# Performance work log

Hardware: AMD Instinct MI355X
Metric: run time of the kernel (lower is better)

The kernel has to match this reference:

```python
import jax, jax.numpy as jnp
import numpy as np


def _leaky(x):
    return jnp.where(x > 0, x, 0.2 * x)


def _time_warp(x, strength, k_wp, k_sh):
    # Vectorized equivalent of the per-sample python loop in _apply_time_warp.
    B, L, Fd = x.shape
    warp_steps = (L * 0.1 * strength).astype(jnp.int32)
    wp = jax.random.randint(k_wp, (B, 1), warp_steps, L - warp_steps)
    sh = jax.random.randint(k_sh, (B, 1), -warp_steps, warp_steps + 1)
    t = jnp.arange(L)[None, :]
    # shift > 0: warped[t] = x[min(t+shift, L-1)] for t >= warp_point, else x[t]
    pos = jnp.where(t >= wp, jnp.minimum(t + sh, L - 1), t)
    # shift < 0: warped[t] = x[t - shift] for warp_point+shift <= t < L+shift, else x[t]
    neg = jnp.where((t >= wp + sh) & (t < L + sh), t - sh, t)
    idx = jnp.where(sh > 0, pos, jnp.where(sh < 0, neg, t))  # (B, L)
    warped = x[jnp.arange(B)[:, None], idx]  # gather along time -> (B, L, Fd)
    return warped


def _freq_aug(x, strength, k_f):
    fx = jnp.fft.fft(x, axis=1)
    ratio = jnp.minimum(strength * 0.1, 0.5)
    keep = jax.random.uniform(k_f, x.shape) > ratio
    res = jnp.fft.ifft(fx * keep.astype(fx.dtype), axis=1).real.astype(x.dtype)
    return jnp.where(strength < 0.01, x, res)


def _forward(x, batch_size, w1, b1, w2, b2, w3, b3, wm, bm, wn, bn, ws, bs,
             p_mask, p_noise, p_shift, p_scale):
    B, L, Fd = x.shape
    s_mask = jax.nn.sigmoid(p_mask)
    s_noise = jax.nn.sigmoid(p_noise)
    s_shift = jax.nn.sigmoid(p_shift)
    s_scale = jax.nn.sigmoid(p_scale)
    s_mix = 1.0 - s_shift

    key = jax.random.key(42)
    kz, kn, kwp, ksh, kf = jax.random.split(key, 5)

    z = jax.random.normal(kz, (B, w1.shape[0]), x.dtype)
    h = _leaky(z @ w1 + b1)
    h = _leaky(h @ w2 + b2)
    h = _leaky(h @ w3 + b3)  # (B, 2*hidden)

    mask = jax.nn.sigmoid(h @ wm + bm).reshape(B, L, Fd)
    mask = 1.0 - (1.0 - mask) * s_mask * 0.3

    noise_mag = jax.nn.softplus(h @ wn + bn).reshape(B, L, Fd)
    noise = jax.random.normal(kn, x.shape, x.dtype) * noise_mag * s_noise * 0.05

    warped = _time_warp(x, s_shift, kwp, ksh)

    scale = jax.nn.softplus(h @ ws + bs)[:, None, :]  # (B,1,Fd)
    scale = 1.0 + (scale - 0.5) * 0.2 * s_scale

    freq = _freq_aug(x, s_mix, kf)

    wa = jnp.clip(1.0 - s_mix - s_shift, 0.1, 0.8)
    wb = s_mix * 0.5
    wc = s_shift * 0.5
    tot = wa + wb + wc
    wa, wb, wc = wa / tot, wb / tot, wc / tot

    aug = x * mask * scale + noise
    aug = aug * wa + freq * wb + warped * wc
    return aug


def setup_inputs() -> dict:
    key = jax.random.key(0)
    ks = jax.random.split(key, 8)
    B, L, Fd = 256, 512, 64
    H, ND = 128, 64
    x = jax.random.normal(ks[0], (B, L, Fd), jnp.float32)

    def lin(k, i, o):
        return jax.random.normal(k, (i, o), jnp.float32) * 0.02

    inp = {
        "x": x,
        "batch_size": B,
        "w1": lin(ks[1], ND, H), "b1": jnp.zeros((H,), jnp.float32),
        "w2": lin(ks[2], H, 2 * H), "b2": jnp.zeros((2 * H,), jnp.float32),
        "w3": lin(ks[3], 2 * H, 2 * H), "b3": jnp.zeros((2 * H,), jnp.float32),
        "wm": lin(ks[4], 2 * H, L * Fd), "bm": jnp.zeros((L * Fd,), jnp.float32),
        "wn": lin(ks[5], 2 * H, L * Fd), "bn": jnp.zeros((L * Fd,), jnp.float32),
        "ws": lin(ks[6], 2 * H, Fd), "bs": jnp.zeros((Fd,), jnp.float32),
        "p_mask": jnp.float32(0.5), "p_noise": jnp.float32(0.5),
        "p_shift": jnp.float32(0.5), "p_scale": jnp.float32(0.5),
    }
    return inp


def reference(x, batch_size, w1, b1, w2, b2, w3, b3, wm, bm, wn, bn, ws, bs,
              p_mask, p_noise, p_shift, p_scale):
    return _forward(x, batch_size, w1, b1, w2, b2, w3, b3, wm, bm, wn, bn,
                    ws, bs, p_mask, p_noise, p_shift, p_scale)
```

## Files before the change

### kernel.cpp

```cpp
#include <hip/hip_runtime.h>
#include <cstdint>
#include <cstddef>


typedef unsigned int u32;
typedef unsigned short u16;

#define Bd 256
#define Ld 512
#define Fd 64
#define Nd 32768

struct U2 { u32 a, b; };

__device__ __forceinline__ u32 rotl32(u32 x, int r){ return (x << r) | (x >> (32 - r)); }

__device__ __forceinline__ U2 tf2x32(u32 k0, u32 k1, u32 x0, u32 x1){
  u32 ks2 = k0 ^ k1 ^ 0x1BD11BDAu;
  x0 += k0; x1 += k1;
#define TFR4(r0,r1,r2,r3) \
  x0 += x1; x1 = rotl32(x1, r0); x1 ^= x0; \
  x0 += x1; x1 = rotl32(x1, r1); x1 ^= x0; \
  x0 += x1; x1 = rotl32(x1, r2); x1 ^= x0; \
  x0 += x1; x1 = rotl32(x1, r3); x1 ^= x0;
  TFR4(13,15,26,6)  x0 += k1;  x1 += ks2 + 1u;
  TFR4(17,29,16,24) x0 += ks2; x1 += k0 + 2u;
  TFR4(13,15,26,6)  x0 += k0;  x1 += k1 + 3u;
  TFR4(17,29,16,24) x0 += k1;  x1 += ks2 + 4u;
  TFR4(13,15,26,6)  x0 += ks2; x1 += k0 + 5u;
#undef TFR4
  U2 r; r.a = x0; r.b = x1; return r;
}

__device__ __forceinline__ u32 rb32(u32 k0, u32 k1, u32 i){
  U2 r = tf2x32(k0, k1, 0u, i);
  return r.a ^ r.b;
}

__device__ __forceinline__ U2 split_key(u32 k0, u32 k1, u32 j){
  return tf2x32(k0, k1, 0u, j);
}

__device__ __forceinline__ float sigmoidf_(float x){ return 1.0f / (1.0f + expf(-x)); }
__device__ __forceinline__ float softplusf_(float x){ return fmaxf(x, 0.0f) + log1pf(expf(-fabsf(x))); }
__device__ __forceinline__ float leakyf_(float x){ return (x > 0.0f) ? x : 0.2f * x; }

__device__ __forceinline__ float erfinvf_(float x){
  float w = -log1pf(-x * x);
  float p;
  if (w < 5.0f){
    w -= 2.5f;
    p =               2.81022636e-08f;
    p = fmaf(p, w,    3.43273939e-07f);
    p = fmaf(p, w,   -3.5233877e-06f);
    p = fmaf(p, w,   -4.39150654e-06f);
    p = fmaf(p, w,    0.00021858087f);
    p = fmaf(p, w,   -0.00125372503f);
    p = fmaf(p, w,   -0.00417768164f);
    p = fmaf(p, w,    0.246640727f);
    p = fmaf(p, w,    1.50140941f);
  } else {
    w = sqrtf(w) - 3.0f;
    p =              -0.000200214257f;
    p = fmaf(p, w,    0.000100950558f);
    p = fmaf(p, w,    0.00134934322f);
    p = fmaf(p, w,   -0.00367342844f);
    p = fmaf(p, w,    0.00573950773f);
    p = fmaf(p, w,   -0.0076224613f);
    p = fmaf(p, w,    0.00943887047f);
    p = fmaf(p, w,    1.00167406f);
    p = fmaf(p, w,    2.83297682f);
  }
  return p * x;
}

__device__ __forceinline__ float uniform_from_bits(u32 bits){
  return __uint_as_float((bits >> 9) | 0x3f800000u) - 1.0f;
}

__device__ __forceinline__ float normal_from_bits(u32 bits){
  float u01 = uniform_from_bits(bits);
  const float lo = -0.99999994f;
  float v = fmaf(u01, 2.0f, lo);
  v = fmaxf(lo, v);
  return 1.41421356f * erfinvf_(v);
}

__device__ __forceinline__ int warp_idx_(int t, int wp, int sh){
  int tps = t + sh;
  int pos = (t >= wp) ? ((tps < Ld - 1) ? tps : (Ld - 1)) : t;
  int neg = ((t >= wp + sh) && (t < Ld + sh)) ? (t - sh) : t;
  return (sh > 0) ? pos : ((sh < 0) ? neg : t);
}

__device__ __forceinline__ u32 pack_bf16_2(float a, float b){
  u32 ua = __float_as_uint(a), ub = __float_as_uint(b);
  u32 ra = (ua + 0x7FFFu + ((ua >> 16) & 1u)) >> 16;
  u32 rb = (ub + 0x7FFFu + ((ub >> 16) & 1u)) >> 16;
  return (ra & 0xFFFFu) | (rb << 16);
}
__device__ __forceinline__ u16 f2bf(float a){
  u32 ua = __float_as_uint(a);
  return (u16)((ua + 0x7FFFu + ((ua >> 16) & 1u)) >> 16);
}
__device__ __forceinline__ float bf2f(u16 v){
  return __uint_as_float(((u32)v) << 16);
}

__device__ __forceinline__ int swz_(int v){
  return ((v >> 2) & 7) ^ ((v & 3) << 1);
}
__device__ __forceinline__ int rev9_(int k){
  return (int)(__brev((u32)k) >> 23);
}

__global__ __launch_bounds__(256) void k_mlp(
    const float* __restrict__ w1, const float* __restrict__ b1,
    const float* __restrict__ w2, const float* __restrict__ b2,
    const float* __restrict__ w3, const float* __restrict__ b3,
    const float* __restrict__ wsc, const float* __restrict__ bsc,
    const float* __restrict__ p_scale, const float* __restrict__ p_shift,
    u16* __restrict__ h3b, float* __restrict__ scl,
    int* __restrict__ wp, int* __restrict__ shv)
{
  __shared__ float zs[64];
  __shared__ float h1s[128];
  __shared__ float h2s[256];
  __shared__ float hs[256];
  int b = blockIdx.x, n = threadIdx.x;

  if (n < 64){
    U2 kz = split_key(0u, 42u, 0u);
    zs[n] = normal_from_bits(rb32(kz.a, kz.b, (u32)(b * 64 + n)));
  }
  __syncthreads();

  if (n < 128){
    float acc = b1[n];
    #pragma unroll 8
    for (int k = 0; k < 64; ++k) acc = fmaf(zs[k], w1[k * 128 + n], acc);
    h1s[n] = leakyf_(acc);
  }
  __syncthreads();

  {
    float acc = b2[n];
    #pragma unroll 8
    for (int k = 0; k < 128; ++k) acc = fmaf(h1s[k], w2[k * 256 + n], acc);
    h2s[n] = leakyf_(acc);
  }
  __syncthreads();

  {
    float acc = b3[n];
    #pragma unroll 8
    for (int k = 0; k < 256; ++k) acc = fmaf(h2s[k], w3[k * 256 + n], acc);
    u16 hv = f2bf(leakyf_(acc));
    h3b[b * 256 + n] = hv;
    hs[n] = bf2f(hv);
  }
  __syncthreads();

  if (n < 64){
    float a2 = bsc[n];
    for (int k = 0; k < 256; ++k) a2 = fmaf(hs[k], wsc[k * 64 + n], a2);
    float s_scale = sigmoidf_(p_scale[0]);
    scl[b * 64 + n] = 1.0f + (softplusf_(a2) - 0.5f) * 0.2f * s_scale;
  }

  if (b < 2 && n < 128){
    int bb = b * 128 + n;
    float s_shift = sigmoidf_(p_shift[0]);
    int wsteps = (int)(51.2f * s_shift);
    U2 kwp = split_key(0u, 42u, 2u);
    U2 ksh = split_key(0u, 42u, 3u);
    {
      U2 k1 = split_key(kwp.a, kwp.b, 0u);
      U2 k2 = split_key(kwp.a, kwp.b, 1u);
      u32 hi = rb32(k1.a, k1.b, (u32)bb);
      u32 lo = rb32(k2.a, k2.b, (u32)bb);
      u32 span = (u32)(Ld - 2 * wsteps);
      u32 mult = 65536u % span; mult = (mult * mult) % span;
      u32 off = ((hi % span) * mult + (lo % span)) % span;
      wp[bb] = wsteps + (int)off;
    }
    {
      U2 k1 = split_key(ksh.a, ksh.b, 0u);
      U2 k2 = split_key(ksh.a, ksh.b, 1u);
      u32 hi = rb32(k1.a, k1.b, (u32)bb);
      u32 lo = rb32(k2.a, k2.b, (u32)bb);
      u32 span = (u32)(2 * wsteps + 1);
      u32 mult = 65536u % span; mult = (mult * mult) % span;
      u32 off = ((hi % span) * mult + (lo % span)) % span;
      shv[bb] = -wsteps + (int)off;
    }
  }
}

typedef short short8 __attribute__((ext_vector_type(8)));
typedef float f32x4 __attribute__((ext_vector_type(4)));
union Frag { uint4 u; short8 s; };

__global__ __launch_bounds__(256, 2) void k_gemm(
    const u16* __restrict__ h3b,
    const float* __restrict__ wm, const float* __restrict__ bm,
    const float* __restrict__ wn, const float* __restrict__ bn,
    u32* __restrict__ mn)
{
  __shared__ __align__(16) u32 As [128 * 32];
  __shared__ __align__(16) u32 Bs0[128 * 32];
  __shared__ __align__(16) u32 Bs1[128 * 32];

  const int tid  = threadIdx.x;
  const int lane = tid & 63;
  const int w    = tid >> 6;
  const int q    = lane >> 4;
  const int lo   = lane & 15;
  const int nt0  = blockIdx.x << 7;
  const int b0   = blockIdx.y << 7;
  const int wr   = (w >> 1) << 6;
  const int wc   = (w & 1) << 6;

  const int p  = lane >> 3;
  const int c8 = lane & 7;
  const int nb = (w << 5) + (p << 2);

  f32x4 accm[4][4], accn[4][4];
  #pragma unroll
  for (int i = 0; i < 4; ++i)
    #pragma unroll
    for (int j = 0; j < 4; ++j){ accm[i][j] = (f32x4)0.0f; accn[i][j] = (f32x4)0.0f; }

  for (int kc = 0; kc < 256; kc += 64){
    if (kc) __syncthreads();
    #pragma unroll
    for (int j = 0; j < 4; ++j){
      int idx  = j * 256 + tid;
      int row  = idx >> 3;
      int slot = idx & 7;
      int g    = slot ^ swz_(row);
      uint4 v  = *(const uint4*)(h3b + (size_t)(b0 + row) * 256 + kc + g * 8);
      *(uint4*)&As[row * 32 + slot * 4] = v;
    }
    #pragma unroll
    for (int cp = 0; cp < 4; ++cp){
      int c = cp * 8 + c8;
      size_t gb = (size_t)(kc + 2 * c) * Nd + nt0 + nb;
      float4 m0 = *(const float4*)(wm + gb);
      float4 m1 = *(const float4*)(wm + gb + Nd);
      float4 v0 = *(const float4*)(wn + gb);
      float4 v1 = *(const float4*)(wn + gb + Nd);
      int g = c >> 2, cl = c & 3;
      #pragma unroll
      for (int s = 0; s < 4; ++s){
        int n = nb + s;
        int addr = n * 32 + (g ^ swz_(n)) * 4 + cl;
        float a0 = (s == 0) ? m0.x : (s == 1) ? m0.y : (s == 2) ? m0.z : m0.w;
        float a1 = (s == 0) ? m1.x : (s == 1) ? m1.y : (s == 2) ? m1.z : m1.w;
        float b0f = (s == 0) ? v0.x : (s == 1) ? v0.y : (s == 2) ? v0.z : v0.w;
        float b1f = (s == 0) ? v1.x : (s == 1) ? v1.y : (s == 2) ? v1.z : v1.w;
        Bs0[addr] = pack_bf16_2(a0, a1);
        Bs1[addr] = pack_bf16_2(b0f, b1f);
      }
    }
    __syncthreads();

    #pragma unroll
    for (int u = 0; u < 2; ++u){
      int G = u * 4 + q;
      Frag af[4], bfm[4], bfn[4];
      #pragma unroll
      for (int mt = 0; mt < 4; ++mt){
        int row = wr + mt * 16 + lo;
        af[mt].u = *(const uint4*)&As[row * 32 + (G ^ swz_(row)) * 4];
      }
      #pragma unroll
      for (int nt = 0; nt < 4; ++nt){
        int n = wc + nt * 16 + lo;
        int ad = n * 32 + (G ^ swz_(n)) * 4;
        bfm[nt].u = *(const uint4*)&Bs0[ad];
        bfn[nt].u = *(const uint4*)&Bs1[ad];
      }
      #pragma unroll
      for (int mt = 0; mt < 4; ++mt){
        #pragma unroll
        for (int nt = 0; nt < 4; ++nt){
          accm[mt][nt] = __builtin_amdgcn_mfma_f32_16x16x32_bf16(af[mt].s, bfm[nt].s, accm[mt][nt], 0, 0, 0);
          accn[mt][nt] = __builtin_amdgcn_mfma_f32_16x16x32_bf16(af[mt].s, bfn[nt].s, accn[mt][nt], 0, 0, 0);
        }
      }
    }
  }

  #pragma unroll
  for (int nt = 0; nt < 4; ++nt){
    int n = nt0 + wc + nt * 16 + lo;
    float bmv = bm[n];
    float bnv = bn[n];
    #pragma unroll
    for (int mt = 0; mt < 4; ++mt){
      #pragma unroll
      for (int r = 0; r < 4; ++r){
        int b = b0 + wr + mt * 16 + q * 4 + r;
        size_t o = (size_t)b * Nd + n;
        mn[o] = pack_bf16_2(accm[mt][nt][r] + bmv, accn[mt][nt][r] + bnv);
      }
    }
  }
}

__global__ __launch_bounds__(256) void k_noise(u32* __restrict__ mn,
                                               const float* __restrict__ p_noise){
  int gid = blockIdx.x * 256 + threadIdx.x;
  u32 base = (u32)gid * 8u;
  float s_noise = sigmoidf_(p_noise[0]);
  float sc = s_noise * 0.05f;
  U2 knk = split_key(0u, 42u, 1u);

  uint4 v0 = *(const uint4*)(mn + base);
  uint4 v1 = *(const uint4*)(mn + base + 4);
  u32 wds[8] = {v0.x, v0.y, v0.z, v0.w, v1.x, v1.y, v1.z, v1.w};
  #pragma unroll
  for (int h = 0; h < 8; ++h){
    u16 logit = (u16)(wds[h] >> 16);
    float nm = softplusf_(bf2f(logit));
    float nz = normal_from_bits(rb32(knk.a, knk.b, base + (u32)h));
    wds[h] = (wds[h] & 0xFFFFu) | ((u32)f2bf(nz * nm * sc) << 16);
  }
  *(uint4*)(mn + base)     = make_uint4(wds[0], wds[1], wds[2], wds[3]);
  *(uint4*)(mn + base + 4) = make_uint4(wds[4], wds[5], wds[6], wds[7]);
}

#define PITCH 529

__device__ __forceinline__ int lphys(int t){ return t + (t >> 5); }

__global__ __launch_bounds__(256, 4) void k_faug(
    const float* __restrict__ x,
    u32* mn,
    const float* __restrict__ scl,
    const int* __restrict__ wp, const int* __restrict__ shv,
    const float* __restrict__ p_mask, const float* __restrict__ p_noise,
    const float* __restrict__ p_shift)
{
  __shared__ float SR[8 * PITCH];
  __shared__ float SI[8 * PITCH];
  __shared__ float2 tw[256];

  const int tid = threadIdx.x;
  const int b   = blockIdx.x >> 2;
  const int f0  = (blockIdx.x & 3) << 4;

  float s_mask  = sigmoidf_(p_mask[0]);
  float s_shift = sigmoidf_(p_shift[0]);
  float s_mix   = 1.0f - s_shift;
  float ratio   = fminf(s_mix * 0.1f, 0.5f);
  float wa = 1.0f - s_mix - s_shift;
  wa = fminf(fmaxf(wa, 0.1f), 0.8f);
  float wb = s_mix * 0.5f;
  float wc = s_shift * 0.5f;
  float tot = wa + wb + wc;
  wa /= tot; wb /= tot; wc /= tot;
  bool pass = (s_mix < 0.01f);
  (void)p_noise;

  U2 kf  = split_key(0u, 42u, 4u);
  const int wpb = wp[b];
  const int shb = shv[b];

  {
    float ang = -6.283185307179586f * ((float)tid / 512.0f);
    tw[tid] = make_float2(cosf(ang), sinf(ang));
  }

  const float* xb = x + (size_t)b * Nd;
  #pragma unroll
  for (int s = 0; s < 8; ++s){
    int qq = (s << 8) + tid;
    int t  = qq >> 2;
    int f4 = qq & 3;
    float4 v = *(const float4*)(xb + t * 64 + f0 + (f4 << 2));
    int j = f4 << 1;
    int pt = lphys(t);
    SR[j * PITCH + pt]       = v.x;  SI[j * PITCH + pt]       = v.y;
    SR[(j + 1) * PITCH + pt] = v.z;  SI[(j + 1) * PITCH + pt] = v.w;
  }
  __syncthreads();

  for (int s = 9; s >= 1; --s){
    int half = 1 << (s - 1);
    #pragma unroll
    for (int it = 0; it < 8; ++it){
      int j  = it;
      int bi = tid;
      int pos = bi & (half - 1);
      int g = bi >> (s - 1);
      int i1 = (g << s) + pos;
      int i2 = i1 + half;
      int a1 = j * PITCH + lphys(i1);
      int a2 = j * PITCH + lphys(i2);
      float ur = SR[a1], ui = SI[a1];
      float vr = SR[a2], vi = SI[a2];
      SR[a1] = ur + vr; SI[a1] = ui + vi;
      float dr = ur - vr, di = ui - vi;
      float2 w = tw[pos << (9 - s)];
      SR[a2] = dr * w.x - di * w.y;
      SI[a2] = dr * w.y + di * w.x;
    }
    __syncthreads();
  }

  #pragma unroll
  for (int it = 0; it < 8; ++it){
    int j = it;
    int k = tid;
    int nItr = (k == 0) ? 2 : 1;
    for (int e = 0; e < nItr; ++e){
      int kk = (e == 0) ? k : 256;
      int nk = (512 - kk) & 511;
      int pk = rev9_(kk), pn = rev9_(nk);
      int ak = j * PITCH + lphys(pk);
      int an = j * PITCH + lphys(pn);
      float zkr = SR[ak], zki = SI[ak];
      float znr = SR[an], zni = SI[an];
      float X0r = 0.5f * (zkr + znr), X0i = 0.5f * (zki - zni);
      float X1r = 0.5f * (zki + zni), X1i = 0.5f * (znr - zkr);
      int fA = f0 + (j << 1);
      u32 ck = (u32)((b * Ld + kk) * Fd + fA);
      u32 cn = (u32)((b * Ld + nk) * Fd + fA);
      float k0a = (uniform_from_bits(rb32(kf.a, kf.b, ck))      > ratio) ? 1.0f : 0.0f;
      float k0b = (uniform_from_bits(rb32(kf.a, kf.b, cn))      > ratio) ? 1.0f : 0.0f;
      float k1a = (uniform_from_bits(rb32(kf.a, kf.b, ck + 1u)) > ratio) ? 1.0f : 0.0f;
      float k1b = (uniform_from_bits(rb32(kf.a, kf.b, cn + 1u)) > ratio) ? 1.0f : 0.0f;
      float m0 = 0.5f * (k0a + k0b);
      float m1 = 0.5f * (k1a + k1b);
      SR[ak] = m0 * X0r - m1 * X1i;
      SI[ak] = m0 * X0i + m1 * X1r;
      SR[an] = m0 * X0r + m1 * X1i;
      SI[an] = m1 * X1r - m0 * X0i;
    }
  }
  __syncthreads();

  for (int s = 1; s <= 9; ++s){
    int half = 1 << (s - 1);
    #pragma unroll
    for (int it = 0; it < 8; ++it){
      int j  = it;
      int bi = tid;
      int pos = bi & (half - 1);
      int g = bi >> (s - 1);
      int i1 = (g << s) + pos;
      int i2 = i1 + half;
      int a1 = j * PITCH + lphys(i1);
      int a2 = j * PITCH + lphys(i2);
      float2 w = tw[pos << (9 - s)];
      float vr = SR[a2], vi = SI[a2];
      float tx_ = vr * w.x + vi * w.y;
      float ty_ = vi * w.x - vr * w.y;
      float ur = SR[a1], ui = SI[a1];
      SR[a1] = ur + tx_; SI[a1] = ui + ty_;
      SR[a2] = ur - tx_; SI[a2] = ui - ty_;
    }
    __syncthreads();
  }

  const float inv512 = 1.0f / 512.0f;
  u32* mnb = mn + (size_t)b * Nd;
  #pragma unroll
  for (int s = 0; s < 8; ++s){
    int qq = (s << 8) + tid;
    int t  = qq >> 2;
    int f4 = qq & 3;
    int f  = f0 + (f4 << 2);
    int j  = f4 << 1;
    int pt = lphys(t);
    int nidx = t * 64 + f;
    float4 xv = *(const float4*)(xb + nidx);
    int wi = warp_idx_(t, wpb, shb);
    float4 wv = *(const float4*)(xb + wi * 64 + f);
    float4 sc = *(const float4*)(scl + b * 64 + f);
    uint4 w4 = *(const uint4*)(mnb + nidx);
    float fr[4];
    fr[0] = SR[j * PITCH + pt] * inv512;
    fr[1] = SI[j * PITCH + pt] * inv512;
    fr[2] = SR[(j + 1) * PITCH + pt] * inv512;
    fr[3] = SI[(j + 1) * PITCH + pt] * inv512;
    const float xvv[4] = {xv.x, xv.y, xv.z, xv.w};
    const float wvv[4] = {wv.x, wv.y, wv.z, wv.w};
    const float scv[4] = {sc.x, sc.y, sc.z, sc.w};
    const u32 wdv[4] = {w4.x, w4.y, w4.z, w4.w};
    float o[4];
    #pragma unroll
    for (int c = 0; c < 4; ++c){
      float maskv = sigmoidf_(bf2f((u16)(wdv[c] & 0xFFFFu)));
      maskv = 1.0f - (1.0f - maskv) * s_mask * 0.3f;
      float noise = bf2f((u16)(wdv[c] >> 16));
      float fq = pass ? xvv[c] : fr[c];
      float aug = fmaf(xvv[c] * maskv, scv[c], noise);
      o[c] = aug * wa + fq * wb + wvv[c] * wc;
    }
    *(float4*)(mnb + nidx) = make_float4(o[0], o[1], o[2], o[3]);
  }
}

extern "C" void kernel_launch(void* const* d_in, const int* in_sizes, int n_in,
                              void* d_out, int out_size, void* d_ws, size_t ws_size,
                              hipStream_t stream)
{
  (void)in_sizes; (void)n_in; (void)out_size; (void)ws_size;
  const float* x   = (const float*)d_in[0];
  const float* w1  = (const float*)d_in[2];
  const float* b1  = (const float*)d_in[3];
  const float* w2  = (const float*)d_in[4];
  const float* b2  = (const float*)d_in[5];
  const float* w3  = (const float*)d_in[6];
  const float* b3  = (const float*)d_in[7];
  const float* wm  = (const float*)d_in[8];
  const float* bm  = (const float*)d_in[9];
  const float* wn  = (const float*)d_in[10];
  const float* bn  = (const float*)d_in[11];
  const float* wsc = (const float*)d_in[12];
  const float* bsc = (const float*)d_in[13];
  const float* pm  = (const float*)d_in[14];
  const float* pn  = (const float*)d_in[15];
  const float* psh = (const float*)d_in[16];
  const float* psc = (const float*)d_in[17];
  char* ws = (char*)d_ws;

  int*   wp   = (int*)(ws + 0);
  int*   shv  = (int*)(ws + 1024);
  u16*   h3b  = (u16*)(ws + 4096);
  float* scl  = (float*)(ws + 4096 + 131072);
  u32*   mn   = (u32*)d_out;

  k_mlp  <<<dim3(256),     dim3(256), 0, stream>>>(w1, b1, w2, b2, w3, b3,
                                                   wsc, bsc, psc, psh,
                                                   h3b, scl, wp, shv);
  k_gemm <<<dim3(256, 2),  dim3(256), 0, stream>>>(h3b, wm, bm, wn, bn, mn);
  k_noise<<<dim3(4096),    dim3(256), 0, stream>>>(mn, pn);
  k_faug <<<dim3(1024),    dim3(256), 0, stream>>>(x, mn, scl, wp, shv,
                                                   pm, pn, psh);
}
```

Before: 315.3 us.

## Fuse all four kernels into one cooperative persistent kernel with grid syncs

Replaces the four separate launches (MLP, GEMM, noise, frequency augmentation) with a single cooperative kernel. Each phase iterates over its work items with a persistent grid-stride loop, and phases are separated by grid.sync(), with shared memory reused across phases. The goal is to remove launch overhead and inter-kernel gaps. In exchange, occupancy is capped at what a cooperative launch allows, the 1024 FFT tiles and 4096 noise blocks now run on fewer resident blocks, and grid-wide barriers add their own cost.

```diff
diff --git a/kernel.cpp b/kernel.cpp
--- a/kernel.cpp
+++ b/kernel.cpp
@@ -1,6 +1,9 @@
 #include <hip/hip_runtime.h>
+#include <hip/hip_cooperative_groups.h>
 #include <cstdint>
 #include <cstddef>
+
+namespace cg = cooperative_groups;
 
 
 typedef unsigned int u32;
@@ -114,393 +117,401 @@
   return (int)(__brev((u32)k) >> 23);
 }
 
-__global__ __launch_bounds__(256) void k_mlp(
+typedef short short8 __attribute__((ext_vector_type(8)));
+typedef float f32x4 __attribute__((ext_vector_type(4)));
+union Frag { uint4 u; short8 s; };
+
+#define PITCH 529
+__device__ __forceinline__ int lphys(int t){ return t + (t >> 5); }
+
+__global__ __launch_bounds__(256, 2) void k_mega(
+    const float* __restrict__ x,
     const float* __restrict__ w1, const float* __restrict__ b1,
     const float* __restrict__ w2, const float* __restrict__ b2,
     const float* __restrict__ w3, const float* __restrict__ b3,
-    const float* __restrict__ wsc, const float* __restrict__ bsc,
-    const float* __restrict__ p_scale, const float* __restrict__ p_shift,
-    u16* __restrict__ h3b, float* __restrict__ scl,
-    int* __restrict__ wp, int* __restrict__ shv)
-{
-  __shared__ float zs[64];
-  __shared__ float h1s[128];
-  __shared__ float h2s[256];
-  __shared__ float hs[256];
-  int b = blockIdx.x, n = threadIdx.x;
-
-  if (n < 64){
-    U2 kz = split_key(0u, 42u, 0u);
-    zs[n] = normal_from_bits(rb32(kz.a, kz.b, (u32)(b * 64 + n)));
-  }
-  __syncthreads();
-
-  if (n < 128){
-    float acc = b1[n];
-    #pragma unroll 8
-    for (int k = 0; k < 64; ++k) acc = fmaf(zs[k], w1[k * 128 + n], acc);
-    h1s[n] = leakyf_(acc);
-  }
-  __syncthreads();
-
-  {
-    float acc = b2[n];
-    #pragma unroll 8
-    for (int k = 0; k < 128; ++k) acc = fmaf(h1s[k], w2[k * 256 + n], acc);
-    h2s[n] = leakyf_(acc);
-  }
-  __syncthreads();
-
-  {
-    float acc = b3[n];
-    #pragma unroll 8
-    for (int k = 0; k < 256; ++k) acc = fmaf(h2s[k], w3[k * 256 + n], acc);
-    u16 hv = f2bf(leakyf_(acc));
-    h3b[b * 256 + n] = hv;
-    hs[n] = bf2f(hv);
-  }
-  __syncthreads();
-
-  if (n < 64){
-    float a2 = bsc[n];
-    for (int k = 0; k < 256; ++k) a2 = fmaf(hs[k], wsc[k * 64 + n], a2);
-    float s_scale = sigmoidf_(p_scale[0]);
-    scl[b * 64 + n] = 1.0f + (softplusf_(a2) - 0.5f) * 0.2f * s_scale;
-  }
-
-  if (b < 2 && n < 128){
-    int bb = b * 128 + n;
-    float s_shift = sigmoidf_(p_shift[0]);
-    int wsteps = (int)(51.2f * s_shift);
-    U2 kwp = split_key(0u, 42u, 2u);
-    U2 ksh = split_key(0u, 42u, 3u);
-    {
-      U2 k1 = split_key(kwp.a, kwp.b, 0u);
-      U2 k2 = split_key(kwp.a, kwp.b, 1u);
-      u32 hi = rb32(k1.a, k1.b, (u32)bb);
-      u32 lo = rb32(k2.a, k2.b, (u32)bb);
-      u32 span = (u32)(Ld - 2 * wsteps);
-      u32 mult = 65536u % span; mult = (mult * mult) % span;
-      u32 off = ((hi % span) * mult + (lo % span)) % span;
-      wp[bb] = wsteps + (int)off;
-    }
-    {
-      U2 k1 = split_key(ksh.a, ksh.b, 0u);
-      U2 k2 = split_key(ksh.a, ksh.b, 1u);
-      u32 hi = rb32(k1.a, k1.b, (u32)bb);
-      u32 lo = rb32(k2.a, k2.b, (u32)bb);
-      u32 span = (u32)(2 * wsteps + 1);
-      u32 mult = 65536u % span; mult = (mult * mult) % span;
-      u32 off = ((hi % span) * mult + (lo % span)) % span;
-      shv[bb] = -wsteps + (int)off;
-    }
-  }
-}
-
-typedef short short8 __attribute__((ext_vector_type(8)));
-typedef float f32x4 __attribute__((ext_vector_type(4)));
-union Frag { uint4 u; short8 s; };
-
-__global__ __launch_bounds__(256, 2) void k_gemm(
-    const u16* __restrict__ h3b,
     const float* __restrict__ wm, const float* __restrict__ bm,
     const float* __restrict__ wn, const float* __restrict__ bn,
-    u32* __restrict__ mn)
+    const float* __restrict__ wsc, const float* __restrict__ bsc,
+    const float* __restrict__ pm, const float* __restrict__ pn,
+    const float* __restrict__ psh, const float* __restrict__ psc,
+    u16* __restrict__ h3b, float* __restrict__ scl,
+    int* __restrict__ wp, int* __restrict__ shv,
+    u32* mn)
 {
-  __shared__ __align__(16) u32 As [128 * 32];
-  __shared__ __align__(16) u32 Bs0[128 * 32];
-  __shared__ __align__(16) u32 Bs1[128 * 32];
-
-  const int tid  = threadIdx.x;
-  const int lane = tid & 63;
-  const int w    = tid >> 6;
-  const int q    = lane >> 4;
-  const int lo   = lane & 15;
-  const int nt0  = blockIdx.x << 7;
-  const int b0   = blockIdx.y << 7;
-  const int wr   = (w >> 1) << 6;
-  const int wc   = (w & 1) << 6;
-
-  const int p  = lane >> 3;
-  const int c8 = lane & 7;
-  const int nb = (w << 5) + (p << 2);
-
-  f32x4 accm[4][4], accn[4][4];
-  #pragma unroll
-  for (int i = 0; i < 4; ++i)
-    #pragma unroll
-    for (int j = 0; j < 4; ++j){ accm[i][j] = (f32x4)0.0f; accn[i][j] = (f32x4)0.0f; }
-
-  for (int kc = 0; kc < 256; kc += 64){
-    if (kc) __syncthreads();
-    #pragma unroll
-    for (int j = 0; j < 4; ++j){
-      int idx  = j * 256 + tid;
-      int row  = idx >> 3;
-      int slot = idx & 7;
-      int g    = slot ^ swz_(row);
-      uint4 v  = *(const uint4*)(h3b + (size_t)(b0 + row) * 256 + kc + g * 8);
-      *(uint4*)&As[row * 32 + slot * 4] = v;
-    }
-    #pragma unroll
-    for (int cp = 0; cp < 4; ++cp){
-      int c = cp * 8 + c8;
-      size_t gb = (size_t)(kc + 2 * c) * Nd + nt0 + nb;
-      float4 m0 = *(const float4*)(wm + gb);
-      float4 m1 = *(const float4*)(wm + gb + Nd);
-      float4 v0 = *(const float4*)(wn + gb);
-      float4 v1 = *(const float4*)(wn + gb + Nd);
-      int g = c >> 2, cl = c & 3;
+  cg::grid_group grid = cg::this_grid();
+  __shared__ __align__(16) u32 SMEM[12288];
+
+  const int bid = blockIdx.x;
+  const int tid = threadIdx.x;
+  const int gsz = gridDim.x;
+
+  for (int b = bid; b < 256; b += gsz){
+    float* zs  = (float*)SMEM;
+    float* h1s = zs + 64;
+    float* h2s = h1s + 128;
+    float* hs  = h2s + 256;
+    int n = tid;
+    __syncthreads();
+
+    if (n < 64){
+      U2 kz = split_key(0u, 42u, 0u);
+      zs[n] = normal_from_bits(rb32(kz.a, kz.b, (u32)(b * 64 + n)));
+    }
+    __syncthreads();
+
+    if (n < 128){
+      float acc = b1[n];
+      #pragma unroll 8
+      for (int k = 0; k < 64; ++k) acc = fmaf(zs[k], w1[k * 128 + n], acc);
+      h1s[n] = leakyf_(acc);
+    }
+    __syncthreads();
+
+    {
+      float acc = b2[n];
+      #pragma unroll 8
+      for (int k = 0; k < 128; ++k) acc = fmaf(h1s[k], w2[k * 256 + n], acc);
+      h2s[n] = leakyf_(acc);
+    }
+    __syncthreads();
+
+    {
+      float acc = b3[n];
+      #pragma unroll 8
+      for (int k = 0; k < 256; ++k) acc = fmaf(h2s[k], w3[k * 256 + n], acc);
+      u16 hv = f2bf(leakyf_(acc));
+      h3b[b * 256 + n] = hv;
+      hs[n] = bf2f(hv);
+    }
+    __syncthreads();
+
+    if (n < 64){
+      float a2 = bsc[n];
+      for (int k = 0; k < 256; ++k) a2 = fmaf(hs[k], wsc[k * 64 + n], a2);
+      float s_scale = sigmoidf_(psc[0]);
+      scl[b * 64 + n] = 1.0f + (softplusf_(a2) - 0.5f) * 0.2f * s_scale;
+    }
+
+    if (b < 2 && n < 128){
+      int bb = b * 128 + n;
+      float s_shift = sigmoidf_(psh[0]);
+      int wsteps = (int)(51.2f * s_shift);
+      U2 kwp = split_key(0u, 42u, 2u);
+      U2 ksh = split_key(0u, 42u, 3u);
+      {
+        U2 k1 = split_key(kwp.a, kwp.b, 0u);
+        U2 k2 = split_key(kwp.a, kwp.b, 1u);
+        u32 hi = rb32(k1.a, k1.b, (u32)bb);
+        u32 lo = rb32(k2.a, k2.b, (u32)bb);
+        u32 span = (u32)(Ld - 2 * wsteps);
+        u32 mult = 65536u % span; mult = (mult * mult) % span;
+        u32 off = ((hi % span) * mult + (lo % span)) % span;
+        wp[bb] = wsteps + (int)off;
+      }
+      {
+        U2 k1 = split_key(ksh.a, ksh.b, 0u);
+        U2 k2 = split_key(ksh.a, ksh.b, 1u);
+        u32 hi = rb32(k1.a, k1.b, (u32)bb);
+        u32 lo = rb32(k2.a, k2.b, (u32)bb);
+        u32 span = (u32)(2 * wsteps + 1);
+        u32 mult = 65536u % span; mult = (mult * mult) % span;
+        u32 off = ((hi % span) * mult + (lo % span)) % span;
+        shv[bb] = -wsteps + (int)off;
+      }
+    }
+  }
+  grid.sync();
+
+  {
+    u32* As  = SMEM;
+    u32* Bs0 = SMEM + 4096;
+    u32* Bs1 = SMEM + 8192;
+
+    const int lane = tid & 63;
+    const int w    = tid >> 6;
+    const int q    = lane >> 4;
+    const int lo   = lane & 15;
+    const int wr   = (w >> 1) << 6;
+    const int wc   = (w & 1) << 6;
+
+    const int p  = lane >> 3;
+    const int c8 = lane & 7;
+    const int nb = (w << 5) + (p << 2);
+
+    for (int tile = bid; tile < 512; tile += gsz){
+      const int nt0 = (tile & 255) << 7;
+      const int b0  = (tile >> 8) << 7;
+
+      f32x4 accm[4][4], accn[4][4];
       #pragma unroll
-      for (int s = 0; s < 4; ++s){
-        int n = nb + s;
-        int addr = n * 32 + (g ^ swz_(n)) * 4 + cl;
-        float a0 = (s == 0) ? m0.x : (s == 1) ? m0.y : (s == 2) ? m0.z : m0.w;
-        float a1 = (s == 0) ? m1.x : (s == 1) ? m1.y : (s == 2) ? m1.z : m1.w;
-        float b0f = (s == 0) ? v0.x : (s == 1) ? v0.y : (s == 2) ? v0.z : v0.w;
-        float b1f = (s == 0) ? v1.x : (s == 1) ? v1.y : (s == 2) ? v1.z : v1.w;
-        Bs0[addr] = pack_bf16_2(a0, a1);
-        Bs1[addr] = pack_bf16_2(b0f, b1f);
-      }
-    }
-    __syncthreads();
-
-    #pragma unroll
-    for (int u = 0; u < 2; ++u){
-      int G = u * 4 + q;
-      Frag af[4], bfm[4], bfn[4];
-      #pragma unroll
-      for (int mt = 0; mt < 4; ++mt){
-        int row = wr + mt * 16 + lo;
-        af[mt].u = *(const uint4*)&As[row * 32 + (G ^ swz_(row)) * 4];
-      }
+      for (int i = 0; i < 4; ++i)
+        #pragma unroll
+        for (int j = 0; j < 4; ++j){ accm[i][j] = (f32x4)0.0f; accn[i][j] = (f32x4)0.0f; }
+
+      for (int kc = 0; kc < 256; kc += 64){
+        __syncthreads();
+        #pragma unroll
+        for (int j = 0; j < 4; ++j){
+          int idx  = j * 256 + tid;
+          int row  = idx >> 3;
+          int slot = idx & 7;
+          int g    = slot ^ swz_(row);
+          uint4 v  = *(const uint4*)(h3b + (size_t)(b0 + row) * 256 + kc + g * 8);
+          *(uint4*)&As[row * 32 + slot * 4] = v;
+        }
+        #pragma unroll
+        for (int cp = 0; cp < 4; ++cp){
+          int c = cp * 8 + c8;
+          size_t gb = (size_t)(kc + 2 * c) * Nd + nt0 + nb;
+          float4 m0 = *(const float4*)(wm + gb);
+          float4 m1 = *(const float4*)(wm + gb + Nd);
+          float4 v0 = *(const float4*)(wn + gb);
+          float4 v1 = *(const float4*)(wn + gb + Nd);
+          int g = c >> 2, cl = c & 3;
+          #pragma unroll
+          for (int s = 0; s < 4; ++s){
+            int n = nb + s;
+            int addr = n * 32 + (g ^ swz_(n)) * 4 + cl;
+            float a0 = (s == 0) ? m0.x : (s == 1) ? m0.y : (s == 2) ? m0.z : m0.w;
+            float a1 = (s == 0) ? m1.x : (s == 1) ? m1.y : (s == 2) ? m1.z : m1.w;
+            float b0f = (s == 0) ? v0.x : (s == 1) ? v0.y : (s == 2) ? v0.z : v0.w;
+            float b1f = (s == 0) ? v1.x : (s == 1) ? v1.y : (s == 2) ? v1.z : v1.w;
+            Bs0[addr] = pack_bf16_2(a0, a1);
+            Bs1[addr] = pack_bf16_2(b0f, b1f);
+          }
+        }
+        __syncthreads();
+
+        #pragma unroll
+        for (int u = 0; u < 2; ++u){
+          int G = u * 4 + q;
+          Frag af[4], bfm[4], bfn[4];
+          #pragma unroll
+          for (int mt = 0; mt < 4; ++mt){
+            int row = wr + mt * 16 + lo;
+            af[mt].u = *(const uint4*)&As[row * 32 + (G ^ swz_(row)) * 4];
+          }
+          #pragma unroll
+          for (int nt = 0; nt < 4; ++nt){
+            int n = wc + nt * 16 + lo;
+            int ad = n * 32 + (G ^ swz_(n)) * 4;
+            bfm[nt].u = *(const uint4*)&Bs0[ad];
+            bfn[nt].u = *(const uint4*)&Bs1[ad];
+          }
+          #pragma unroll
+          for (int mt = 0; mt < 4; ++mt){
+            #pragma unroll
+            for (int nt = 0; nt < 4; ++nt){
+              accm[mt][nt] = __builtin_amdgcn_mfma_f32_16x16x32_bf16(af[mt].s, bfm[nt].s, accm[mt][nt], 0, 0, 0);
+              accn[mt][nt] = __builtin_amdgcn_mfma_f32_16x16x32_bf16(af[mt].s, bfn[nt].s, accn[mt][nt], 0, 0, 0);
+            }
+          }
+        }
+      }
+
       #pragma unroll
       for (int nt = 0; nt < 4; ++nt){
-        int n = wc + nt * 16 + lo;
-        int ad = n * 32 + (G ^ swz_(n)) * 4;
-        bfm[nt].u = *(const uint4*)&Bs0[ad];
-        bfn[nt].u = *(const uint4*)&Bs1[ad];
-      }
+        int n = nt0 + wc + nt * 16 + lo;
+        float bmv = bm[n];
+        float bnv = bn[n];
+        #pragma unroll
+        for (int mt = 0; mt < 4; ++mt){
+          #pragma unroll
+          for (int r = 0; r < 4; ++r){
+            int b = b0 + wr + mt * 16 + q * 4 + r;
+            size_t o = (size_t)b * Nd + n;
+            mn[o] = pack_bf16_2(accm[mt][nt][r] + bmv, accn[mt][nt][r] + bnv);
+          }
+        }
+      }
+    }
+  }
+  grid.sync();
+
+  {
+    float s_noise = sigmoidf_(pn[0]);
+    float sc = s_noise * 0.05f;
+    U2 knk = split_key(0u, 42u, 1u);
+    for (int nb2 = bid; nb2 < 4096; nb2 += gsz){
+      int gid = nb2 * 256 + tid;
+      u32 base = (u32)gid * 8u;
+      uint4 v0 = *(const uint4*)(mn + base);
+      uint4 v1 = *(const uint4*)(mn + base + 4);
+      u32 wds[8] = {v0.x, v0.y, v0.z, v0.w, v1.x, v1.y, v1.z, v1.w};
       #pragma unroll
-      for (int mt = 0; mt < 4; ++mt){
-        #pragma unroll
-        for (int nt = 0; nt < 4; ++nt){
-          accm[mt][nt] = __builtin_amdgcn_mfma_f32_16x16x32_bf16(af[mt].s, bfm[nt].s, accm[mt][nt], 0, 0, 0);
-          accn[mt][nt] = __builtin_amdgcn_mfma_f32_16x16x32_bf16(af[mt].s, bfn[nt].s, accn[mt][nt], 0, 0, 0);
-        }
-      }
+      for (int h = 0; h < 8; ++h){
+        u16 logit = (u16)(wds[h] >> 16);
+        float nm = softplusf_(bf2f(logit));
+        float nz = normal_from_bits(rb32(knk.a, knk.b, base + (u32)h));
+        wds[h] = (wds[h] & 0xFFFFu) | ((u32)f2bf(nz * nm * sc) << 16);
+      }
+      *(uint4*)(mn + base)     = make_uint4(wds[0], wds[1], wds[2], wds[3]);
+      *(uint4*)(mn + base + 4) = make_uint4(wds[4], wds[5], wds[6], wds[7]);
     }
   }
-
-  #pragma unroll
-  for (int nt = 0; nt < 4; ++nt){
-    int n = nt0 + wc + nt * 16 + lo;
-    float bmv = bm[n];
-    float bnv = bn[n];
-    #pragma unroll
-    for (int mt = 0; mt < 4; ++mt){
+  grid.sync();
+
+  {
+    float*  SR = (float*)SMEM;
+    float*  SI = SR + 8 * PITCH;
+    float2* tw = (float2*)(SI + 8 * PITCH);
+
+    float s_mask  = sigmoidf_(pm[0]);
+    float s_shift = sigmoidf_(psh[0]);
+    float s_mix   = 1.0f - s_shift;
+    float ratio   = fminf(s_mix * 0.1f, 0.5f);
+    float wa = 1.0f - s_mix - s_shift;
+    wa = fminf(fmaxf(wa, 0.1f), 0.8f);
+    float wb = s_mix * 0.5f;
+    float wc = s_shift * 0.5f;
+    float tot = wa + wb + wc;
+    wa /= tot; wb /= tot; wc /= tot;
+    bool pass = (s_mix < 0.01f);
+
+    U2 kf = split_key(0u, 42u, 4u);
+
+    {
+      float ang = -6.283185307179586f * ((float)tid / 512.0f);
+      tw[tid] = make_float2(cosf(ang), sinf(ang));
+    }
+
+    for (int tile = bid; tile < 1024; tile += gsz){
+      const int b  = tile >> 2;
+      const int f0 = (tile & 3) << 4;
+      const int wpb = wp[b];
+      const int shb = shv[b];
+      __syncthreads();
+
+      const float* xb = x + (size_t)b * Nd;
       #pragma unroll
-      for (int r = 0; r < 4; ++r){
-        int b = b0 + wr + mt * 16 + q * 4 + r;
-        size_t o = (size_t)b * Nd + n;
-        mn[o] = pack_bf16_2(accm[mt][nt][r] + bmv, accn[mt][nt][r] + bnv);
-      }
-    }
-  }
-}
-
-__global__ __launch_bounds__(256) void k_noise(u32* __restrict__ mn,
-                                               const float* __restrict__ p_noise){
-  int gid = blockIdx.x * 256 + threadIdx.x;
-  u32 base = (u32)gid * 8u;
-  float s_noise = sigmoidf_(p_noise[0]);
-  float sc = s_noise * 0.05f;
-  U2 knk = split_key(0u, 42u, 1u);
-
-  uint4 v0 = *(const uint4*)(mn + base);
-  uint4 v1 = *(const uint4*)(mn + base + 4);
-  u32 wds[8] = {v0.x, v0.y, v0.z, v0.w, v1.x, v1.y, v1.z, v1.w};
-  #pragma unroll
-  for (int h = 0; h < 8; ++h){
-    u16 logit = (u16)(wds[h] >> 16);
-    float nm = softplusf_(bf2f(logit));
-    float nz = normal_from_bits(rb32(knk.a, knk.b, base + (u32)h));
-    wds[h] = (wds[h] & 0xFFFFu) | ((u32)f2bf(nz * nm * sc) << 16);
-  }
-  *(uint4*)(mn + base)     = make_uint4(wds[0], wds[1], wds[2], wds[3]);
-  *(uint4*)(mn + base + 4) = make_uint4(wds[4], wds[5], wds[6], wds[7]);
-}
-
-#define PITCH 529
-
-__device__ __forceinline__ int lphys(int t){ return t + (t >> 5); }
-
-__global__ __launch_bounds__(256, 4) void k_faug(
-    const float* __restrict__ x,
-    u32* mn,
-    const float* __restrict__ scl,
-    const int* __restrict__ wp, const int* __restrict__ shv,
-    const float* __restrict__ p_mask, const float* __restrict__ p_noise,
-    const float* __restrict__ p_shift)
-{
-  __shared__ float SR[8 * PITCH];
-  __shared__ float SI[8 * PITCH];
-  __shared__ float2 tw[256];
-
-  const int tid = threadIdx.x;
-  const int b   = blockIdx.x >> 2;
-  const int f0  = (blockIdx.x & 3) << 4;
-
-  float s_mask  = sigmoidf_(p_mask[0]);
-  float s_shift = sigmoidf_(p_shift[0]);
-  float s_mix   = 1.0f - s_shift;
-  float ratio   = fminf(s_mix * 0.1f, 0.5f);
-  float wa = 1.0f - s_mix - s_shift;
-  wa = fminf(fmaxf(wa, 0.1f), 0.8f);
-  float wb = s_mix * 0.5f;
-  float wc = s_shift * 0.5f;
-  float tot = wa + wb + wc;
-  wa /= tot; wb /= tot; wc /= tot;
-  bool pass = (s_mix < 0.01f);
-  (void)p_noise;
-
-  U2 kf  = split_key(0u, 42u, 4u);
-  const int wpb = wp[b];
-  const int shb = shv[b];
-
-  {
-    float ang = -6.283185307179586f * ((float)tid / 512.0f);
-    tw[tid] = make_float2(cosf(ang), sinf(ang));
-  }
-
-  const float* xb = x + (size_t)b * Nd;
-  #pragma unroll
-  for (int s = 0; s < 8; ++s){
-    int qq = (s << 8) + tid;
-    int t  = qq >> 2;
-    int f4 = qq & 3;
-    float4 v = *(const float4*)(xb + t * 64 + f0 + (f4 << 2));
-    int j = f4 << 1;
-    int pt = lphys(t);
-    SR[j * PITCH + pt]       = v.x;  SI[j * PITCH + pt]       = v.y;
-    SR[(j + 1) * PITCH + pt] = v.z;  SI[(j + 1) * PITCH + pt] = v.w;
-  }
-  __syncthreads();
-
-  for (int s = 9; s >= 1; --s){
-    int half = 1 << (s - 1);
-    #pragma unroll
-    for (int it = 0; it < 8; ++it){
-      int j  = it;
-      int bi = tid;
-      int pos = bi & (half - 1);
-      int g = bi >> (s - 1);
-      int i1 = (g << s) + pos;
-      int i2 = i1 + half;
-      int a1 = j * PITCH + lphys(i1);
-      int a2 = j * PITCH + lphys(i2);
-      float ur = SR[a1], ui = SI[a1];
-      float vr = SR[a2], vi = SI[a2];
-      SR[a1] = ur + vr; SI[a1] = ui + vi;
-      float dr = ur - vr, di = ui - vi;
-      float2 w = tw[pos << (9 - s)];
-      SR[a2] = dr * w.x - di * w.y;
-      SI[a2] = dr * w.y + di * w.x;
-    }
-    __syncthreads();
-  }
-
-  #pragma unroll
-  for (int it = 0; it < 8; ++it){
-    int j = it;
-    int k = tid;
-    int nItr = (k == 0) ? 2 : 1;
-    for (int e = 0; e < nItr; ++e){
-      int kk = (e == 0) ? k : 256;
-      int nk = (512 - kk) & 511;
-      int pk = rev9_(kk), pn = rev9_(nk);
-      int ak = j * PITCH + lphys(pk);
-      int an = j * PITCH + lphys(pn);
-      float zkr = SR[ak], zki = SI[ak];
-      float znr = SR[an], zni = SI[an];
-      float X0r = 0.5f * (zkr + znr), X0i = 0.5f * (zki - zni);
-      float X1r = 0.5f * (zki + zni), X1i = 0.5f * (znr - zkr);
-      int fA = f0 + (j << 1);
-      u32 ck = (u32)((b * Ld + kk) * Fd + fA);
-      u32 cn = (u32)((b * Ld + nk) * Fd + fA);
-      float k0a = (uniform_from_bits(rb32(kf.a, kf.b, ck))      > ratio) ? 1.0f : 0.0f;
-      float k0b = (uniform_from_bits(rb32(kf.a, kf.b, cn))      > ratio) ? 1.0f : 0.0f;
-      float k1a = (uniform_from_bits(rb32(kf.a, kf.b, ck + 1u)) > ratio) ? 1.0f : 0.0f;
-      float k1b = (uniform_from_bits(rb32(kf.a, kf.b, cn + 1u)) > ratio) ? 1.0f : 0.0f;
-      float m0 = 0.5f * (k0a + k0b);
-      float m1 = 0.5f * (k1a + k1b);
-      SR[ak] = m0 * X0r - m1 * X1i;
-      SI[ak] = m0 * X0i + m1 * X1r;
-      SR[an] = m0 * X0r + m1 * X1i;
-      SI[an] = m1 * X1r - m0 * X0i;
-    }
-  }
-  __syncthreads();
-
-  for (int s = 1; s <= 9; ++s){
-    int half = 1 << (s - 1);
-    #pragma unroll
-    for (int it = 0; it < 8; ++it){
-      int j  = it;
-      int bi = tid;
-      int pos = bi & (half - 1);
-      int g = bi >> (s - 1);
-      int i1 = (g << s) + pos;
-      int i2 = i1 + half;
-      int a1 = j * PITCH + lphys(i1);
-      int a2 = j * PITCH + lphys(i2);
-      float2 w = tw[pos << (9 - s)];
-      float vr = SR[a2], vi = SI[a2];
-      float tx_ = vr * w.x + vi * w.y;
-      float ty_ = vi * w.x - vr * w.y;
-      float ur = SR[a1], ui = SI[a1];
-      SR[a1] = ur + tx_; SI[a1] = ui + ty_;
-      SR[a2] = ur - tx_; SI[a2] = ui - ty_;
-    }
-    __syncthreads();
-  }
-
-  const float inv512 = 1.0f / 512.0f;
-  u32* mnb = mn + (size_t)b * Nd;
-  #pragma unroll
-  for (int s = 0; s < 8; ++s){
-    int qq = (s << 8) + tid;
-    int t  = qq >> 2;
-    int f4 = qq & 3;
-    int f  = f0 + (f4 << 2);
-    int j  = f4 << 1;
-    int pt = lphys(t);
-    int nidx = t * 64 + f;
-    float4 xv = *(const float4*)(xb + nidx);
-    int wi = warp_idx_(t, wpb, shb);
-    float4 wv = *(const float4*)(xb + wi * 64 + f);
-    float4 sc = *(const float4*)(scl + b * 64 + f);
-    uint4 w4 = *(const uint4*)(mnb + nidx);
-    float fr[4];
-    fr[0] = SR[j * PITCH + pt] * inv512;
-    fr[1] = SI[j * PITCH + pt] * inv512;
-    fr[2] = SR[(j + 1) * PITCH + pt] * inv512;
-    fr[3] = SI[(j + 1) * PITCH + pt] * inv512;
-    const float xvv[4] = {xv.x, xv.y, xv.z, xv.w};
-    const float wvv[4] = {wv.x, wv.y, wv.z, wv.w};
-    const float scv[4] = {sc.x, sc.y, sc.z, sc.w};
-    const u32 wdv[4] = {w4.x, w4.y, w4.z, w4.w};
-    float o[4];
-    #pragma unroll
-    for (int c = 0; c < 4; ++c){
-      float maskv = sigmoidf_(bf2f((u16)(wdv[c] & 0xFFFFu)));
-      maskv = 1.0f - (1.0f - maskv) * s_mask * 0.3f;
-      float noise = bf2f((u16)(wdv[c] >> 16));
-      float fq = pass ? xvv[c] : fr[c];
-      float aug = fmaf(xvv[c] * maskv, scv[c], noise);
-      o[c] = aug * wa + fq * wb + wvv[c] * wc;
-    }
-    *(float4*)(mnb + nidx) = make_float4(o[0], o[1], o[2], o[3]);
+      for (int s = 0; s < 8; ++s){
+        int qq = (s << 8) + tid;
+        int t  = qq >> 2;
+        int f4 = qq & 3;
+        float4 v = *(const float4*)(xb + t * 64 + f0 + (f4 << 2));
+        int j = f4 << 1;
+        int pt = lphys(t);
+        SR[j * PITCH + pt]       = v.x;  SI[j * PITCH + pt]       = v.y;
+        SR[(j + 1) * PITCH + pt] = v.z;  SI[(j + 1) * PITCH + pt] = v.w;
+      }
+      __syncthreads();
+
+      for (int s = 9; s >= 1; --s){
+        int half = 1 << (s - 1);
+        #pragma unroll
+        for (int it = 0; it < 8; ++it){
+          int j  = it;
+          int bi = tid;
+          int pos = bi & (half - 1);
+          int g = bi >> (s - 1);
+          int i1 = (g << s) + pos;
+          int i2 = i1 + half;
+          int a1 = j * PITCH + lphys(i1);
+          int a2 = j * PITCH + lphys(i2);
+          float ur = SR[a1], ui = SI[a1];
+          float vr = SR[a2], vi = SI[a2];
+          SR[a1] = ur + vr; SI[a1] = ui + vi;
+          float dr = ur - vr, di = ui - vi;
+          float2 w = tw[pos << (9 - s)];
+          SR[a2] = dr * w.x - di * w.y;
+          SI[a2] = dr * w.y + di * w.x;
+        }
+        __syncthreads();
+      }
+
+      #pragma unroll
+      for (int it = 0; it < 8; ++it){
+        int j = it;
+        int k = tid;
+        int nItr = (k == 0) ? 2 : 1;
+        for (int e = 0; e < nItr; ++e){
+          int kk = (e == 0) ? k : 256;
+          int nk = (512 - kk) & 511;
+          int pk = rev9_(kk), pnn = rev9_(nk);
+          int ak = j * PITCH + lphys(pk);
+          int an = j * PITCH + lphys(pnn);
+          float zkr = SR[ak], zki = SI[ak];
+          float znr = SR[an], zni = SI[an];
+          float X0r = 0.5f * (zkr + znr), X0i = 0.5f * (zki - zni);
+          float X1r = 0.5f * (zki + zni), X1i = 0.5f * (znr - zkr);
+          int fA = f0 + (j << 1);
+          u32 ck = (u32)((b * Ld + kk) * Fd + fA);
+          u32 cn = (u32)((b * Ld + nk) * Fd + fA);
+          float k0a = (uniform_from_bits(rb32(kf.a, kf.b, ck))      > ratio) ? 1.0f : 0.0f;
+          float k0b = (uniform_from_bits(rb32(kf.a, kf.b, cn))      > ratio) ? 1.0f : 0.0f;
+          float k1a = (uniform_from_bits(rb32(kf.a, kf.b, ck + 1u)) > ratio) ? 1.0f : 0.0f;
+          float k1b = (uniform_from_bits(rb32(kf.a, kf.b, cn + 1u)) > ratio) ? 1.0f : 0.0f;
+          float m0 = 0.5f * (k0a + k0b);
+          float m1 = 0.5f * (k1a + k1b);
+          SR[ak] = m0 * X0r - m1 * X1i;
+          SI[ak] = m0 * X0i + m1 * X1r;
+          SR[an] = m0 * X0r + m1 * X1i;
+          SI[an] = m1 * X1r - m0 * X0i;
+        }
+      }
+      __syncthreads();
+
+      for (int s = 1; s <= 9; ++s){
+        int half = 1 << (s - 1);
+        #pragma unroll
+        for (int it = 0; it < 8; ++it){
+          int j  = it;
+          int bi = tid;
+          int pos = bi & (half - 1);
+          int g = bi >> (s - 1);
+          int i1 = (g << s) + pos;
+          int i2 = i1 + half;
+          int a1 = j * PITCH + lphys(i1);
+          int a2 = j * PITCH + lphys(i2);
+          float2 w = tw[pos << (9 - s)];
+          float vr = SR[a2], vi = SI[a2];
+          float tx_ = vr * w.x + vi * w.y;
+          float ty_ = vi * w.x - vr * w.y;
+          float ur = SR[a1], ui = SI[a1];
+          SR[a1] = ur + tx_; SI[a1] = ui + ty_;
+          SR[a2] = ur - tx_; SI[a2] = ui - ty_;
+        }
+        __syncthreads();
+      }
+
+      const float inv512 = 1.0f / 512.0f;
+      u32* mnb = mn + (size_t)b * Nd;
+      #pragma unroll
+      for (int s = 0; s < 8; ++s){
+        int qq = (s << 8) + tid;
+        int t  = qq >> 2;
+        int f4 = qq & 3;
+        int f  = f0 + (f4 << 2);
+        int j  = f4 << 1;
+        int pt = lphys(t);
+        int nidx = t * 64 + f;
+        float4 xv = *(const float4*)(xb + nidx);
+        int wi = warp_idx_(t, wpb, shb);
+        float4 wv = *(const float4*)(xb + wi * 64 + f);
+        float4 sc = *(const float4*)(scl + b * 64 + f);
+        uint4 w4 = *(const uint4*)(mnb + nidx);
+        float fr[4];
+        fr[0] = SR[j * PITCH + pt] * inv512;
+        fr[1] = SI[j * PITCH + pt] * inv512;
+        fr[2] = SR[(j + 1) * PITCH + pt] * inv512;
+        fr[3] = SI[(j + 1) * PITCH + pt] * inv512;
+        const float xvv[4] = {xv.x, xv.y, xv.z, xv.w};
+        const float wvv[4] = {wv.x, wv.y, wv.z, wv.w};
+        const float scv[4] = {sc.x, sc.y, sc.z, sc.w};
+        const u32 wdv[4] = {w4.x, w4.y, w4.z, w4.w};
+        float o[4];
+        #pragma unroll
+        for (int c = 0; c < 4; ++c){
+          float maskv = sigmoidf_(bf2f((u16)(wdv[c] & 0xFFFFu)));
+          maskv = 1.0f - (1.0f - maskv) * s_mask * 0.3f;
+          float noise = bf2f((u16)(wdv[c] >> 16));
+          float fq = pass ? xvv[c] : fr[c];
+          float aug = fmaf(xvv[c] * maskv, scv[c], noise);
+          o[c] = aug * wa + fq * wb + wvv[c] * wc;
+        }
+        *(float4*)(mnb + nidx) = make_float4(o[0], o[1], o[2], o[3]);
+      }
+    }
   }
 }
 
@@ -534,11 +545,25 @@
   float* scl  = (float*)(ws + 4096 + 131072);
   u32*   mn   = (u32*)d_out;
 
-  k_mlp  <<<dim3(256),     dim3(256), 0, stream>>>(w1, b1, w2, b2, w3, b3,
-                                                   wsc, bsc, psc, psh,
-                                                   h3b, scl, wp, shv);
-  k_gemm <<<dim3(256, 2),  dim3(256), 0, stream>>>(h3b, wm, bm, wn, bn, mn);
-  k_noise<<<dim3(4096),    dim3(256), 0, stream>>>(mn, pn);
-  k_faug <<<dim3(1024),    dim3(256), 0, stream>>>(x, mn, scl, wp, shv,
-                                                   pm, pn, psh);
-}
+  static int coopGrid = 0;
+  if (coopGrid == 0){
+    int perCU = 0;
+    hipError_t e = hipOccupancyMaxActiveBlocksPerMultiprocessor(
+        &perCU, (const void*)k_mega, 256, 0);
+    if (e != hipSuccess || perCU < 1) perCU = 1;
+    long total = (long)perCU * 256;
+    if (total > 512) total = 512;
+    if (total < 1)   total = 1;
+    coopGrid = (int)total;
+  }
+
+  void* args[] = {
+    (void*)&x,  (void*)&w1, (void*)&b1, (void*)&w2, (void*)&b2,
+    (void*)&w3, (void*)&b3, (void*)&wm, (void*)&bm, (void*)&wn,
+    (void*)&bn, (void*)&wsc,(void*)&bsc,(void*)&pm, (void*)&pn,
+    (void*)&psh,(void*)&psc,(void*)&h3b,(void*)&scl,(void*)&wp,
+    (void*)&shv,(void*)&mn
+  };
+  hipLaunchCooperativeKernel((const void*)k_mega, dim3(coopGrid), dim3(256),
+                             args, 0, stream);
+}
```

Measured after the change: 543.3 us. +72.3%, slower.
